# Kernel tuning notes

Measured on AMD Instinct MI355X. Metric: run time of the kernel, lower is better.

Reference implementation:

```python
import jax, jax.numpy as jnp
import numpy as np

E = 8          # num_experts
D = 512        # embed_dim
FF = 4         # ff_mult
H = D * FF     # hidden
B, N = 4, 2048
TOP_K = 2


def setup_inputs() -> dict:
    key = jax.random.key(0)
    ks = jax.random.split(key, 6)
    tokens = jax.random.normal(ks[0], (B, N, D), dtype=jnp.float32)
    # token-choice top-k routing: logits -> top-2 experts per token
    logits = jax.random.normal(ks[1], (B, N, E), dtype=jnp.float32)
    topv, topi = jax.lax.top_k(logits, TOP_K)            # (B,N,K)
    disp = jnp.zeros((B, N, E), jnp.float32)
    disp = jnp.take_along_axis(disp, topi, axis=-1)  # placeholder shape trick avoided below
    disp = jnp.zeros((B, N, E), jnp.float32).at[
        jnp.arange(B)[:, None, None], jnp.arange(N)[None, :, None], topi
    ].set(1.0)                                            # (B,N,E) 0/1 dispatch mask
    w = jax.nn.softmax(topv, axis=-1)                     # combine weights over selected
    comb = jnp.zeros((B, N, E), jnp.float32).at[
        jnp.arange(B)[:, None, None], jnp.arange(N)[None, :, None], topi
    ].set(w)
    # expert params (xavier-ish scale); out_proj gain 0.02 as in module init
    Wg = jax.random.normal(ks[2], (E, D, H), dtype=jnp.float32) * (2.0 / (D + H)) ** 0.5
    Wv = jax.random.normal(ks[3], (E, D, H), dtype=jnp.float32) * (2.0 / (D + H)) ** 0.5
    Wo = jax.random.normal(ks[4], (E, H, D), dtype=jnp.float32) * 0.02 * (2.0 / (D + H)) ** 0.5
    scales = jnp.full((E,), 1.0 / E, dtype=jnp.float32)   # output_scale per expert
    return {"tokens": tokens, "dispatch_weights": disp, "combine_weights": comb,
            "Wg": Wg, "Wv": Wv, "Wo": Wo, "scales": scales}


def reference(tokens, dispatch_weights, combine_weights, Wg, Wv, Wo, scales):
    """ExpertPool.forward: per-expert SwiGLU FFN, combined by routing weights.

    Dense-masked formulation (same math as gather->FFN->weighted scatter-add:
    expert outputs only contribute where dispatch>0).
    """
    b, n, d = tokens.shape
    x = tokens.reshape(b * n, d)                          # (M, D)
    gate = jax.nn.gelu(jnp.einsum('md,edh->emh', x, Wg), approximate=False)
    value = jnp.einsum('md,edh->emh', x, Wv)
    out_e = jnp.einsum('emh,ehd->emd', gate * value, Wo) * scales[:, None, None]
    mask = dispatch_weights.reshape(b * n, -1) > 0        # (M, E)
    w = jnp.where(mask, combine_weights.reshape(b * n, -1), 0.0)
    out = jnp.einsum('emd,me->md', out_e, w)              # weighted combine
    return out.reshape(b, n, d)
```

## Files before the change

### kernel.cpp

```cpp
#include <hip/hip_runtime.h>
#include <hip/hip_bf16.h>


#define NEXP 8
#define DIM 512
#define HID 2048
#define MTOK 8192
#define PMAX (2*MTOK)
#define TM 128
#define MT 144

typedef __bf16 bf16;
typedef __bf16 bf16x8 __attribute__((ext_vector_type(8)));
typedef float  f32x4  __attribute__((ext_vector_type(4)));

#define WAITVM(N) asm volatile("s_waitcnt vmcnt(" #N ")" ::: "memory")
#define SCHED0    __builtin_amdgcn_sched_barrier(0)
#define BAR       __builtin_amdgcn_s_barrier

__device__ __forceinline__ void gload16(const bf16* g, bf16* l) {
  __builtin_amdgcn_global_load_lds(
      (const __attribute__((address_space(1))) void*)g,
      (__attribute__((address_space(3))) void*)l, 16, 0, 0);
}

__global__ __launch_bounds__(256) void k_cvt_x(const float* __restrict__ in,
                                               bf16* __restrict__ out, int n4) {
  int i = blockIdx.x*256 + threadIdx.x;
  if (i >= n4) return;
  float4 v = ((const float4* __restrict__)in)[i];
  bf16 o[4];
  o[0]=(bf16)v.x; o[1]=(bf16)v.y; o[2]=(bf16)v.z; o[3]=(bf16)v.w;
  *(uint2*)&out[(size_t)i*4] = *(uint2*)o;
}

__global__ __launch_bounds__(256) void k_tcvt2(const float* __restrict__ in0,
                                               const float* __restrict__ in1,
                                               bf16* __restrict__ out0,
                                               bf16* __restrict__ out1, int R, int C) {
  __shared__ __align__(16) bf16 t[64][72];
  const int z = blockIdx.z;
  const int e = z & (NEXP-1);
  const float* __restrict__ pin = ((z < NEXP) ? in0 : in1) + (size_t)e*R*C;
  bf16* __restrict__ pout = ((z < NEXP) ? out0 : out1) + (size_t)e*R*C;
  const int c0 = blockIdx.x*64, r0 = blockIdx.y*64;
  const int tid = threadIdx.x;
  const int rr = tid>>4, cc4 = (tid&15)*4;
#pragma unroll
  for (int i=0;i<4;i++){
    int r = i*16 + rr;
    float4 v = *(const float4*)&pin[(size_t)(r0+r)*C + c0 + cc4];
    t[cc4+0][r]=(bf16)v.x; t[cc4+1][r]=(bf16)v.y;
    t[cc4+2][r]=(bf16)v.z; t[cc4+3][r]=(bf16)v.w;
  }
  __syncthreads();
#pragma unroll
  for (int i=0;i<4;i++){
    int c = i*16 + rr;
    *(uint2*)&pout[(size_t)(c0+c)*R + r0 + cc4] = *(uint2*)&t[c][cc4];
  }
}

__global__ __launch_bounds__(256) void k_count(const float* __restrict__ disp,
                                               int* __restrict__ cnt) {
  __shared__ int lc[NEXP];
  int t = threadIdx.x;
  if (t < NEXP) lc[t] = 0;
  __syncthreads();
  int m = blockIdx.x*256 + t;
  float4 d0 = *(const float4*)&disp[(size_t)m*NEXP];
  float4 d1 = *(const float4*)&disp[(size_t)m*NEXP+4];
  if (d0.x>0.f) atomicAdd(&lc[0],1);
  if (d0.y>0.f) atomicAdd(&lc[1],1);
  if (d0.z>0.f) atomicAdd(&lc[2],1);
  if (d0.w>0.f) atomicAdd(&lc[3],1);
  if (d1.x>0.f) atomicAdd(&lc[4],1);
  if (d1.y>0.f) atomicAdd(&lc[5],1);
  if (d1.z>0.f) atomicAdd(&lc[6],1);
  if (d1.w>0.f) atomicAdd(&lc[7],1);
  __syncthreads();
  if (t < NEXP) atomicAdd(&cnt[t], lc[t]);
}

__global__ void k_scan(const int* __restrict__ cnt, int* __restrict__ base,
                       int* __restrict__ te, int* __restrict__ trow, int* __restrict__ tn) {
  __shared__ int sb[NEXP+1], st[NEXP+1], sc[NEXP];
  if (threadIdx.x == 0){
    int b=0, t=0;
    for (int e=0;e<NEXP;e++){
      sb[e]=b; st[e]=t; sc[e]=cnt[e]; base[e]=b;
      b += sc[e];
      t += (sc[e]+TM-1)/TM;
    }
    sb[NEXP]=b; st[NEXP]=t;
  }
  __syncthreads();
  for (int idx=threadIdx.x; idx<MT; idx+=blockDim.x){
    int e=-1;
#pragma unroll
    for (int q=0;q<NEXP;q++) if (idx>=st[q] && idx<st[q+1]) e=q;
    if (e>=0){
      int k = idx - st[e];
      int nr = sc[e] - k*TM; if (nr>TM) nr=TM;
      te[idx]=e; trow[idx]=sb[e]+k*TM; tn[idx]=nr;
    } else te[idx]=-1;
  }
}

__global__ __launch_bounds__(256) void k_fill(const float* __restrict__ disp,
    const float* __restrict__ comb, const float* __restrict__ scales,
    const int* __restrict__ base, int* __restrict__ fillc,
    int* __restrict__ stok, float* __restrict__ sw, int* __restrict__ sslot) {
  int m = blockIdx.x*256 + threadIdx.x;
  int jj = 0;
#pragma unroll
  for (int e=0;e<NEXP;e++){
    float dv = disp[(size_t)m*NEXP + e];
    if (dv > 0.f) {
      int s = atomicAdd(&fillc[e], 1);
      int g = base[e] + s;
      stok[g] = m;
      sw[g] = comb[(size_t)m*NEXP + e] * scales[e];
      if (jj < 2) sslot[m*2 + jj] = g;
      jj++;
    }
  }
}

__global__ __launch_bounds__(256) void k_gemm1(const bf16* __restrict__ Xb,
    const bf16* __restrict__ WgT, const bf16* __restrict__ WvT,
    const int* __restrict__ te, const int* __restrict__ trow, const int* __restrict__ tn,
    const int* __restrict__ stok, bf16* __restrict__ H1) {
  const int tile = blockIdx.y;
  const int e = te[tile];
  if (e < 0) return;
  const int row0 = trow[tile], nrows = tn[tile];
  const int n0 = blockIdx.x*64;
  __shared__ __align__(16) bf16 Al[2*128*32];
  __shared__ __align__(16) bf16 Bgl[2*64*32];
  __shared__ __align__(16) bf16 Bvl[2*64*32];
  const int tid = threadIdx.x, lane = tid&63;
  const int wr = (tid>>7)&1, wc = (tid>>6)&1;
  const bf16* __restrict__ wg = WgT + (size_t)e*HID*DIM;
  const bf16* __restrict__ wv = WvT + (size_t)e*HID*DIM;

  const bf16* asrc[2];
#pragma unroll
  for (int i=0;i<2;i++){
    int c = i*256 + tid;
    int r = c>>2, qs = (c&3) ^ ((r>>1)&3);
    int gr = (r < nrows) ? (row0 + r) : row0;
    asrc[i] = Xb + (size_t)stok[gr]*DIM + qs*8;
  }
  const bf16 *bsg, *bsv;
  {
    int r = tid>>2, qs = (tid&3) ^ ((r>>1)&3);
    size_t o = (size_t)(n0 + r)*DIM + qs*8;
    bsg = wg + o; bsv = wv + o;
  }
  const int wbase = (tid&192)*8;

  auto stage = [&](int bi, int kt){
    const int k0 = kt*32;
    gload16(asrc[0]+k0, Al + bi*4096 + wbase);
    gload16(asrc[1]+k0, Al + bi*4096 + 2048 + wbase);
    gload16(bsg+k0, Bgl + bi*2048 + wbase);
    gload16(bsv+k0, Bvl + bi*2048 + wbase);
  };

  f32x4 accg[4][2] = {}, accv[4][2] = {};
  const int r15 = lane&15;
  const int koff = ((lane>>4) ^ ((r15>>1)&3))*8;
  stage(0, 0);
  for (int kt=0; kt<DIM/32; ++kt){
    const int bi = kt&1;
    if (kt+1 < DIM/32){ stage(bi^1, kt+1); WAITVM(4); }
    else WAITVM(0);
    BAR(); SCHED0;
    bf16x8 a[4], bg[2], bv[2];
#pragma unroll
    for (int ni=0; ni<2; ni++){
      bg[ni] = *(const bf16x8*)&Bgl[bi*2048 + (wc*32 + ni*16 + r15)*32 + koff];
      bv[ni] = *(const bf16x8*)&Bvl[bi*2048 + (wc*32 + ni*16 + r15)*32 + koff];
    }
#pragma unroll
    for (int mi=0; mi<4; mi++)
      a[mi] = *(const bf16x8*)&Al[bi*4096 + (wr*64 + mi*16 + r15)*32 + koff];
#pragma unroll
    for (int mi=0; mi<4; mi++)
#pragma unroll
      for (int ni=0; ni<2; ni++){
        accg[mi][ni] = __builtin_amdgcn_mfma_f32_16x16x32_bf16(a[mi], bg[ni], accg[mi][ni], 0,0,0);
        accv[mi][ni] = __builtin_amdgcn_mfma_f32_16x16x32_bf16(a[mi], bv[ni], accv[mi][ni], 0,0,0);
      }
    BAR(); SCHED0;
  }
  const int cb = n0 + wc*32 + r15;
  const int rb = wr*64 + (lane>>4)*4;
#pragma unroll
  for (int mi=0; mi<4; mi++)
#pragma unroll
    for (int j=0; j<4; j++){
      int r = rb + mi*16 + j;
      if (r < nrows){
#pragma unroll
        for (int ni=0; ni<2; ni++){
          float g = accg[mi][ni][j], v = accv[mi][ni][j];
          float ge = 0.5f*g*(1.f + erff(g*0.70710678118654752f));
          H1[(size_t)(row0+r)*HID + cb + ni*16] = (bf16)(ge*v);
        }
      }
    }
}

__global__ __launch_bounds__(256) void k_gemm2(const bf16* __restrict__ H1,
    const bf16* __restrict__ WoT,
    const int* __restrict__ te, const int* __restrict__ trow, const int* __restrict__ tn,
    const float* __restrict__ sw, float* __restrict__ gout) {
  const int L = blockIdx.x;
  const int tile = (L&7)*18 + (L>>5);
  const int n0 = ((L>>3)&3)*128;
  const int e = te[tile];
  if (e < 0) return;
  const int row0 = trow[tile], nrows = tn[tile];
  __shared__ __align__(16) bf16 Al[2*TM*64];
  __shared__ __align__(16) bf16 Bl[2*TM*64];
  const int tid = threadIdx.x, lane = tid&63;
  const int wr = (tid>>7)&1, wc = (tid>>6)&1;
  const bf16* __restrict__ wo = WoT + (size_t)e*DIM*HID;

  const bf16 *asrc[4], *bsrc[4];
#pragma unroll
  for (int i=0;i<4;i++){
    int c = i*256 + tid;
    int r = c>>3, qs = (c&7) ^ (r&7);
    int ar = (r < nrows) ? (row0 + r) : row0;
    asrc[i] = H1 + (size_t)ar*HID + qs*8;
    bsrc[i] = wo + (size_t)(n0 + r)*HID + qs*8;
  }
  const int wbase = (tid&192)*8;

  auto stage = [&](int bi, int kt){
    const int k0 = kt*64;
#pragma unroll
    for (int i=0;i<4;i++){
      gload16(asrc[i]+k0, Al + bi*TM*64 + i*2048 + wbase);
      gload16(bsrc[i]+k0, Bl + bi*TM*64 + i*2048 + wbase);
    }
  };

  f32x4 acc[4][4] = {};
  const int rsw = (lane&7)<<3;
  stage(0, 0);
  for (int kt=0; kt<HID/64; ++kt){
    const int bi = kt&1;
    if (kt+1 < HID/64){ stage(bi^1, kt+1); WAITVM(8); }
    else WAITVM(0);
    BAR(); SCHED0;
#pragma unroll
    for (int ks=0; ks<2; ks++){
      const int kos = (ks*32 + (lane>>4)*8) ^ rsw;
      bf16x8 a[4], b[4];
#pragma unroll
      for (int ni=0; ni<4; ni++)
        b[ni] = *(const bf16x8*)&Bl[bi*TM*64 + (wc*64 + ni*16 + (lane&15))*64 + kos];
#pragma unroll
      for (int mi=0; mi<4; mi++)
        a[mi] = *(const bf16x8*)&Al[bi*TM*64 + (wr*64 + mi*16 + (lane&15))*64 + kos];
#pragma unroll
      for (int mi=0; mi<4; mi++)
#pragma unroll
        for (int ni=0; ni<4; ni++)
          acc[mi][ni] = __builtin_amdgcn_mfma_f32_16x16x32_bf16(a[mi], b[ni], acc[mi][ni], 0,0,0);
    }
    BAR(); SCHED0;
  }
  const int cb = n0 + wc*64 + (lane&15);
  const int rb = wr*64 + (lane>>4)*4;
#pragma unroll
  for (int mi=0; mi<4; mi++)
#pragma unroll
    for (int j=0; j<4; j++){
      int r = rb + mi*16 + j;
      if (r < nrows){
        int slot = row0 + r;
        float wgt = sw[slot];
        float* op = gout + (size_t)slot*DIM + cb;
#pragma unroll
        for (int ni=0; ni<4; ni++)
          op[ni*16] = acc[mi][ni][j] * wgt;
      }
    }
}

__global__ __launch_bounds__(256) void k_comb(const float* __restrict__ gout,
    const int* __restrict__ sslot, float* __restrict__ out) {
  int idx = blockIdx.x*256 + threadIdx.x;
  int m = idx >> 7, c4 = (idx & 127)*4;
  int s0 = sslot[m*2], s1 = sslot[m*2+1];
  float4 x = *(const float4*)&gout[(size_t)s0*DIM + c4];
  float4 y = *(const float4*)&gout[(size_t)s1*DIM + c4];
  x.x += y.x; x.y += y.y; x.z += y.z; x.w += y.w;
  *(float4*)&out[(size_t)m*DIM + c4] = x;
}

extern "C" void kernel_launch(void* const* d_in, const int* in_sizes, int n_in,
                              void* d_out, int out_size, void* d_ws, size_t ws_size,
                              hipStream_t stream) {
  const float* tokens = (const float*)d_in[0];
  const float* disp   = (const float*)d_in[1];
  const float* comb   = (const float*)d_in[2];
  const float* Wg     = (const float*)d_in[3];
  const float* Wv     = (const float*)d_in[4];
  const float* Wo     = (const float*)d_in[5];
  const float* scales = (const float*)d_in[6];
  float* out = (float*)d_out;

  size_t off = 0;
  char* wsb = (char*)d_ws;
  auto take = [&](size_t bytes)->char* {
    char* q = wsb + off; off += (bytes + 255) & ~(size_t)255; return q;
  };
  int*   cnt   = (int*)  take(NEXP*4);
  int*   basee = (int*)  take(NEXP*4);
  int*   fillc = (int*)  take(NEXP*4);
  int*   te    = (int*)  take(MT*4);
  int*   trow  = (int*)  take(MT*4);
  int*   tnr   = (int*)  take(MT*4);
  int*   stok  = (int*)  take((size_t)PMAX*4);
  float* sw    = (float*)take((size_t)PMAX*4);
  int*   sslot = (int*)  take((size_t)MTOK*2*4);
  bf16*  Xb    = (bf16*) take((size_t)MTOK*DIM*2);
  bf16*  WgT   = (bf16*) take((size_t)NEXP*DIM*HID*2);
  bf16*  WvT   = (bf16*) take((size_t)NEXP*DIM*HID*2);
  bf16*  WoT   = (bf16*) take((size_t)NEXP*DIM*HID*2);
  bf16*  H1    = (bf16*) take((size_t)PMAX*HID*2);
  float* gout  = (float*)WgT;
  (void)ws_size; (void)in_sizes; (void)n_in; (void)out_size;

  hipMemsetAsync(d_ws, 0, 768, stream);

  k_cvt_x<<<dim3((MTOK*DIM/4)/256), 256, 0, stream>>>(tokens, Xb, MTOK*DIM/4);
  k_tcvt2<<<dim3(HID/64, DIM/64, 2*NEXP), 256, 0, stream>>>(Wg, Wv, WgT, WvT, DIM, HID);
  k_tcvt2<<<dim3(DIM/64, HID/64, NEXP), 256, 0, stream>>>(Wo, Wo, WoT, WoT, HID, DIM);
  k_count<<<dim3(MTOK/256), 256, 0, stream>>>(disp, cnt);
  k_scan <<<1, 64, 0, stream>>>(cnt, basee, te, trow, tnr);
  k_fill <<<dim3(MTOK/256), 256, 0, stream>>>(disp, comb, scales, basee, fillc, stok, sw, sslot);
  k_gemm1<<<dim3(HID/64, MT), 256, 0, stream>>>(Xb, WgT, WvT, te, trow, tnr, stok, H1);
  k_gemm2<<<dim3(8*18*4), 256, 0, stream>>>(H1, WoT, te, trow, tnr, sw, gout);
  k_comb <<<dim3(MTOK*DIM/4/256), 256, 0, stream>>>(gout, sslot, out);
}
```

Measured before the change: 229.7 us.

## Use single-wave 64x32 tiles for gate/value GEMM and polynomial erf GELU

The first expert GEMM now runs one 64-lane wave per block on a 64-row by 32-column tile, so it needs no workgroup barriers, and it gets its own finer tile schedule (TM1=64) separate from the second GEMM's 128-row tiles. The aim is less barrier overhead, less padding waste on partial expert tiles, and more blocks to spread across CUs. The exact erff is replaced by an Abramowitz-Stegun polynomial with __expf, which cuts epilogue cost but carries about 1e-7 absolute erf error. Smaller tiles lower operand reuse, so weight traffic from global memory or L2 goes up.

```diff
diff --git a/kernel.cpp b/kernel.cpp
--- a/kernel.cpp
+++ b/kernel.cpp
@@ -7,8 +7,10 @@
 #define HID 2048
 #define MTOK 8192
 #define PMAX (2*MTOK)
-#define TM 128
-#define MT 144
+#define TM1 64
+#define MT1 264
+#define TM2 128
+#define MT2 144
 
 typedef __bf16 bf16;
 typedef __bf16 bf16x8 __attribute__((ext_vector_type(8)));
@@ -22,6 +24,17 @@
   __builtin_amdgcn_global_load_lds(
       (const __attribute__((address_space(1))) void*)g,
       (__attribute__((address_space(3))) void*)l, 16, 0, 0);
+}
+
+__device__ __forceinline__ float gelu_f(float x){
+  float s = x * 0.70710678118654752f;
+  float a = fabsf(s);
+  float t = 1.0f / fmaf(0.3275911f, a, 1.0f);
+  float p = t*(0.254829592f + t*(-0.284496736f + t*(1.421413741f +
+            t*(-1.453152027f + t*1.061405429f))));
+  float er = 1.0f - p*__expf(-s*s);
+  er = copysignf(er, s);
+  return 0.5f*x*(1.0f + er);
 }
 
 __global__ __launch_bounds__(256) void k_cvt_x(const float* __restrict__ in,
@@ -83,27 +96,39 @@
 }
 
 __global__ void k_scan(const int* __restrict__ cnt, int* __restrict__ base,
-                       int* __restrict__ te, int* __restrict__ trow, int* __restrict__ tn) {
-  __shared__ int sb[NEXP+1], st[NEXP+1], sc[NEXP];
+                       int* __restrict__ te1, int* __restrict__ trow1, int* __restrict__ tn1,
+                       int* __restrict__ te2, int* __restrict__ trow2, int* __restrict__ tn2) {
+  __shared__ int sb[NEXP+1], st1[NEXP+1], st2[NEXP+1], sc[NEXP];
   if (threadIdx.x == 0){
-    int b=0, t=0;
+    int b=0, t1=0, t2=0;
     for (int e=0;e<NEXP;e++){
-      sb[e]=b; st[e]=t; sc[e]=cnt[e]; base[e]=b;
+      sb[e]=b; st1[e]=t1; st2[e]=t2; sc[e]=cnt[e]; base[e]=b;
       b += sc[e];
-      t += (sc[e]+TM-1)/TM;
-    }
-    sb[NEXP]=b; st[NEXP]=t;
+      t1 += (sc[e]+TM1-1)/TM1;
+      t2 += (sc[e]+TM2-1)/TM2;
+    }
+    sb[NEXP]=b; st1[NEXP]=t1; st2[NEXP]=t2;
   }
   __syncthreads();
-  for (int idx=threadIdx.x; idx<MT; idx+=blockDim.x){
+  for (int idx=threadIdx.x; idx<MT1; idx+=blockDim.x){
     int e=-1;
 #pragma unroll
-    for (int q=0;q<NEXP;q++) if (idx>=st[q] && idx<st[q+1]) e=q;
+    for (int q=0;q<NEXP;q++) if (idx>=st1[q] && idx<st1[q+1]) e=q;
     if (e>=0){
-      int k = idx - st[e];
-      int nr = sc[e] - k*TM; if (nr>TM) nr=TM;
-      te[idx]=e; trow[idx]=sb[e]+k*TM; tn[idx]=nr;
-    } else te[idx]=-1;
+      int k = idx - st1[e];
+      int nr = sc[e] - k*TM1; if (nr>TM1) nr=TM1;
+      te1[idx]=e; trow1[idx]=sb[e]+k*TM1; tn1[idx]=nr;
+    } else te1[idx]=-1;
+  }
+  for (int idx=threadIdx.x; idx<MT2; idx+=blockDim.x){
+    int e=-1;
+#pragma unroll
+    for (int q=0;q<NEXP;q++) if (idx>=st2[q] && idx<st2[q+1]) e=q;
+    if (e>=0){
+      int k = idx - st2[e];
+      int nr = sc[e] - k*TM2; if (nr>TM2) nr=TM2;
+      te2[idx]=e; trow2[idx]=sb[e]+k*TM2; tn2[idx]=nr;
+    } else te2[idx]=-1;
   }
 }
 
@@ -127,7 +152,7 @@
   }
 }
 
-__global__ __launch_bounds__(256) void k_gemm1(const bf16* __restrict__ Xb,
+__global__ __launch_bounds__(64) void k_gemm1(const bf16* __restrict__ Xb,
     const bf16* __restrict__ WgT, const bf16* __restrict__ WvT,
     const int* __restrict__ te, const int* __restrict__ trow, const int* __restrict__ tn,
     const int* __restrict__ stok, bf16* __restrict__ H1) {
@@ -135,79 +160,81 @@
   const int e = te[tile];
   if (e < 0) return;
   const int row0 = trow[tile], nrows = tn[tile];
-  const int n0 = blockIdx.x*64;
-  __shared__ __align__(16) bf16 Al[2*128*32];
-  __shared__ __align__(16) bf16 Bgl[2*64*32];
-  __shared__ __align__(16) bf16 Bvl[2*64*32];
-  const int tid = threadIdx.x, lane = tid&63;
-  const int wr = (tid>>7)&1, wc = (tid>>6)&1;
+  const int n0 = blockIdx.x*32;
+  __shared__ __align__(16) bf16 Al[2][2048];
+  __shared__ __align__(16) bf16 Bgl[2][1024];
+  __shared__ __align__(16) bf16 Bvl[2][1024];
+  const int lane = threadIdx.x;
   const bf16* __restrict__ wg = WgT + (size_t)e*HID*DIM;
   const bf16* __restrict__ wv = WvT + (size_t)e*HID*DIM;
 
-  const bf16* asrc[2];
-#pragma unroll
-  for (int i=0;i<2;i++){
-    int c = i*256 + tid;
+  const bf16* asrc[4];
+#pragma unroll
+  for (int i=0;i<4;i++){
+    int c = i*64 + lane;
     int r = c>>2, qs = (c&3) ^ ((r>>1)&3);
     int gr = (r < nrows) ? (row0 + r) : row0;
     asrc[i] = Xb + (size_t)stok[gr]*DIM + qs*8;
   }
-  const bf16 *bsg, *bsv;
-  {
-    int r = tid>>2, qs = (tid&3) ^ ((r>>1)&3);
+  const bf16 *bsg[2], *bsv[2];
+#pragma unroll
+  for (int j=0;j<2;j++){
+    int c = j*64 + lane;
+    int r = c>>2, qs = (c&3) ^ ((r>>1)&3);
     size_t o = (size_t)(n0 + r)*DIM + qs*8;
-    bsg = wg + o; bsv = wv + o;
-  }
-  const int wbase = (tid&192)*8;
+    bsg[j] = wg + o; bsv[j] = wv + o;
+  }
 
   auto stage = [&](int bi, int kt){
     const int k0 = kt*32;
-    gload16(asrc[0]+k0, Al + bi*4096 + wbase);
-    gload16(asrc[1]+k0, Al + bi*4096 + 2048 + wbase);
-    gload16(bsg+k0, Bgl + bi*2048 + wbase);
-    gload16(bsv+k0, Bvl + bi*2048 + wbase);
+#pragma unroll
+    for (int i=0;i<4;i++) gload16(asrc[i]+k0, &Al[bi][i*512]);
+#pragma unroll
+    for (int j=0;j<2;j++){
+      gload16(bsg[j]+k0, &Bgl[bi][j*512]);
+      gload16(bsv[j]+k0, &Bvl[bi][j*512]);
+    }
   };
 
-  f32x4 accg[4][2] = {}, accv[4][2] = {};
+  f32x4 ag[4][2] = {}, av[4][2] = {};
   const int r15 = lane&15;
   const int koff = ((lane>>4) ^ ((r15>>1)&3))*8;
+
   stage(0, 0);
   for (int kt=0; kt<DIM/32; ++kt){
     const int bi = kt&1;
-    if (kt+1 < DIM/32){ stage(bi^1, kt+1); WAITVM(4); }
+    if (kt+1 < DIM/32){ stage(bi^1, kt+1); WAITVM(8); }
     else WAITVM(0);
-    BAR(); SCHED0;
+    SCHED0;
     bf16x8 a[4], bg[2], bv[2];
 #pragma unroll
     for (int ni=0; ni<2; ni++){
-      bg[ni] = *(const bf16x8*)&Bgl[bi*2048 + (wc*32 + ni*16 + r15)*32 + koff];
-      bv[ni] = *(const bf16x8*)&Bvl[bi*2048 + (wc*32 + ni*16 + r15)*32 + koff];
+      bg[ni] = *(const bf16x8*)&Bgl[bi][(ni*16 + r15)*32 + koff];
+      bv[ni] = *(const bf16x8*)&Bvl[bi][(ni*16 + r15)*32 + koff];
     }
 #pragma unroll
     for (int mi=0; mi<4; mi++)
-      a[mi] = *(const bf16x8*)&Al[bi*4096 + (wr*64 + mi*16 + r15)*32 + koff];
+      a[mi] = *(const bf16x8*)&Al[bi][(mi*16 + r15)*32 + koff];
 #pragma unroll
     for (int mi=0; mi<4; mi++)
 #pragma unroll
       for (int ni=0; ni<2; ni++){
-        accg[mi][ni] = __builtin_amdgcn_mfma_f32_16x16x32_bf16(a[mi], bg[ni], accg[mi][ni], 0,0,0);
-        accv[mi][ni] = __builtin_amdgcn_mfma_f32_16x16x32_bf16(a[mi], bv[ni], accv[mi][ni], 0,0,0);
+        ag[mi][ni] = __builtin_amdgcn_mfma_f32_16x16x32_bf16(a[mi], bg[ni], ag[mi][ni], 0,0,0);
+        av[mi][ni] = __builtin_amdgcn_mfma_f32_16x16x32_bf16(a[mi], bv[ni], av[mi][ni], 0,0,0);
       }
-    BAR(); SCHED0;
-  }
-  const int cb = n0 + wc*32 + r15;
-  const int rb = wr*64 + (lane>>4)*4;
+  }
+
+  const int rb = (lane>>4)*4;
 #pragma unroll
   for (int mi=0; mi<4; mi++)
 #pragma unroll
     for (int j=0; j<4; j++){
-      int r = rb + mi*16 + j;
+      int r = mi*16 + rb + j;
       if (r < nrows){
 #pragma unroll
         for (int ni=0; ni<2; ni++){
-          float g = accg[mi][ni][j], v = accv[mi][ni][j];
-          float ge = 0.5f*g*(1.f + erff(g*0.70710678118654752f));
-          H1[(size_t)(row0+r)*HID + cb + ni*16] = (bf16)(ge*v);
+          float g = ag[mi][ni][j], v = av[mi][ni][j];
+          H1[(size_t)(row0+r)*HID + n0 + ni*16 + r15] = (bf16)(gelu_f(g)*v);
         }
       }
     }
@@ -223,8 +250,8 @@
   const int e = te[tile];
   if (e < 0) return;
   const int row0 = trow[tile], nrows = tn[tile];
-  __shared__ __align__(16) bf16 Al[2*TM*64];
-  __shared__ __align__(16) bf16 Bl[2*TM*64];
+  __shared__ __align__(16) bf16 Al[2*TM2*64];
+  __shared__ __align__(16) bf16 Bl[2*TM2*64];
   const int tid = threadIdx.x, lane = tid&63;
   const int wr = (tid>>7)&1, wc = (tid>>6)&1;
   const bf16* __restrict__ wo = WoT + (size_t)e*DIM*HID;
@@ -244,8 +271,8 @@
     const int k0 = kt*64;
 #pragma unroll
     for (int i=0;i<4;i++){
-      gload16(asrc[i]+k0, Al + bi*TM*64 + i*2048 + wbase);
-      gload16(bsrc[i]+k0, Bl + bi*TM*64 + i*2048 + wbase);
+      gload16(asrc[i]+k0, Al + bi*TM2*64 + i*2048 + wbase);
+      gload16(bsrc[i]+k0, Bl + bi*TM2*64 + i*2048 + wbase);
     }
   };
 
@@ -263,10 +290,10 @@
       bf16x8 a[4], b[4];
 #pragma unroll
       for (int ni=0; ni<4; ni++)
-        b[ni] = *(const bf16x8*)&Bl[bi*TM*64 + (wc*64 + ni*16 + (lane&15))*64 + kos];
+        b[ni] = *(const bf16x8*)&Bl[bi*TM2*64 + (wc*64 + ni*16 + (lane&15))*64 + kos];
 #pragma unroll
       for (int mi=0; mi<4; mi++)
-        a[mi] = *(const bf16x8*)&Al[bi*TM*64 + (wr*64 + mi*16 + (lane&15))*64 + kos];
+        a[mi] = *(const bf16x8*)&Al[bi*TM2*64 + (wr*64 + mi*16 + (lane&15))*64 + kos];
 #pragma unroll
       for (int mi=0; mi<4; mi++)
 #pragma unroll
@@ -324,9 +351,12 @@
   int*   cnt   = (int*)  take(NEXP*4);
   int*   basee = (int*)  take(NEXP*4);
   int*   fillc = (int*)  take(NEXP*4);
-  int*   te    = (int*)  take(MT*4);
-  int*   trow  = (int*)  take(MT*4);
-  int*   tnr   = (int*)  take(MT*4);
+  int*   te1   = (int*)  take(MT1*4);
+  int*   trow1 = (int*)  take(MT1*4);
+  int*   tn1   = (int*)  take(MT1*4);
+  int*   te2   = (int*)  take(MT2*4);
+  int*   trow2 = (int*)  take(MT2*4);
+  int*   tn2   = (int*)  take(MT2*4);
   int*   stok  = (int*)  take((size_t)PMAX*4);
   float* sw    = (float*)take((size_t)PMAX*4);
   int*   sslot = (int*)  take((size_t)MTOK*2*4);
@@ -344,9 +374,9 @@
   k_tcvt2<<<dim3(HID/64, DIM/64, 2*NEXP), 256, 0, stream>>>(Wg, Wv, WgT, WvT, DIM, HID);
   k_tcvt2<<<dim3(DIM/64, HID/64, NEXP), 256, 0, stream>>>(Wo, Wo, WoT, WoT, HID, DIM);
   k_count<<<dim3(MTOK/256), 256, 0, stream>>>(disp, cnt);
-  k_scan <<<1, 64, 0, stream>>>(cnt, basee, te, trow, tnr);
+  k_scan <<<1, 64, 0, stream>>>(cnt, basee, te1, trow1, tn1, te2, trow2, tn2);
   k_fill <<<dim3(MTOK/256), 256, 0, stream>>>(disp, comb, scales, basee, fillc, stok, sw, sslot);
-  k_gemm1<<<dim3(HID/64, MT), 256, 0, stream>>>(Xb, WgT, WvT, te, trow, tnr, stok, H1);
-  k_gemm2<<<dim3(8*18*4), 256, 0, stream>>>(H1, WoT, te, trow, tnr, sw, gout);
+  k_gemm1<<<dim3(HID/32, MT1), 64, 0, stream>>>(Xb, WgT, WvT, te1, trow1, tn1, stok, H1);
+  k_gemm2<<<dim3(8*18*4), 256, 0, stream>>>(H1, WoT, te2, trow2, tn2, sw, gout);
   k_comb <<<dim3(MTOK*DIM/4/256), 256, 0, stream>>>(gout, sslot, out);
 }
```

Result: slower. 274.9 us (+19.7%).

## Remap gemm1 grid to interleave expert tiles, shrink gemm2 K-step to 32

Applied to the files above, without the earlier changes.

gemm1 now uses a 1-D grid whose block index is decoded so that consecutive blocks cycle across 8 tile groups, with the N-column index in the middle bits. The aim is to spread concurrently running blocks across experts and XCDs for better L2 reuse of weights. gemm2 switches from a 64-wide K stage to a 32-wide one, with matching swizzle and half the LDS per buffer. That should raise occupancy, at the cost of twice as many barriers and loop iterations.

```diff
diff --git a/kernel.cpp b/kernel.cpp
--- a/kernel.cpp
+++ b/kernel.cpp
@@ -131,11 +131,12 @@
     const bf16* __restrict__ WgT, const bf16* __restrict__ WvT,
     const int* __restrict__ te, const int* __restrict__ trow, const int* __restrict__ tn,
     const int* __restrict__ stok, bf16* __restrict__ H1) {
-  const int tile = blockIdx.y;
+  const int L = blockIdx.x;
+  const int tile = (L&7)*18 + (L>>8);
+  const int n0 = ((L>>3)&31)*64;
   const int e = te[tile];
   if (e < 0) return;
   const int row0 = trow[tile], nrows = tn[tile];
-  const int n0 = blockIdx.x*64;
   __shared__ __align__(16) bf16 Al[2*128*32];
   __shared__ __align__(16) bf16 Bgl[2*64*32];
   __shared__ __align__(16) bf16 Bvl[2*64*32];
@@ -223,17 +224,17 @@
   const int e = te[tile];
   if (e < 0) return;
   const int row0 = trow[tile], nrows = tn[tile];
-  __shared__ __align__(16) bf16 Al[2*TM*64];
-  __shared__ __align__(16) bf16 Bl[2*TM*64];
+  __shared__ __align__(16) bf16 Al[2*128*32];
+  __shared__ __align__(16) bf16 Bl[2*128*32];
   const int tid = threadIdx.x, lane = tid&63;
   const int wr = (tid>>7)&1, wc = (tid>>6)&1;
   const bf16* __restrict__ wo = WoT + (size_t)e*DIM*HID;
 
-  const bf16 *asrc[4], *bsrc[4];
-#pragma unroll
-  for (int i=0;i<4;i++){
+  const bf16 *asrc[2], *bsrc[2];
+#pragma unroll
+  for (int i=0;i<2;i++){
     int c = i*256 + tid;
-    int r = c>>3, qs = (c&7) ^ (r&7);
+    int r = c>>2, qs = (c&3) ^ ((r>>1)&3);
     int ar = (r < nrows) ? (row0 + r) : row0;
     asrc[i] = H1 + (size_t)ar*HID + qs*8;
     bsrc[i] = wo + (size_t)(n0 + r)*HID + qs*8;
@@ -241,41 +242,38 @@
   const int wbase = (tid&192)*8;
 
   auto stage = [&](int bi, int kt){
-    const int k0 = kt*64;
-#pragma unroll
-    for (int i=0;i<4;i++){
-      gload16(asrc[i]+k0, Al + bi*TM*64 + i*2048 + wbase);
-      gload16(bsrc[i]+k0, Bl + bi*TM*64 + i*2048 + wbase);
+    const int k0 = kt*32;
+#pragma unroll
+    for (int i=0;i<2;i++){
+      gload16(asrc[i]+k0, Al + bi*4096 + i*2048 + wbase);
+      gload16(bsrc[i]+k0, Bl + bi*4096 + i*2048 + wbase);
     }
   };
 
   f32x4 acc[4][4] = {};
-  const int rsw = (lane&7)<<3;
+  const int r15 = lane&15;
+  const int koff = ((lane>>4) ^ ((r15>>1)&3))*8;
   stage(0, 0);
-  for (int kt=0; kt<HID/64; ++kt){
+  for (int kt=0; kt<HID/32; ++kt){
     const int bi = kt&1;
-    if (kt+1 < HID/64){ stage(bi^1, kt+1); WAITVM(8); }
+    if (kt+1 < HID/32){ stage(bi^1, kt+1); WAITVM(4); }
     else WAITVM(0);
     BAR(); SCHED0;
-#pragma unroll
-    for (int ks=0; ks<2; ks++){
-      const int kos = (ks*32 + (lane>>4)*8) ^ rsw;
-      bf16x8 a[4], b[4];
+    bf16x8 a[4], b[4];
+#pragma unroll
+    for (int ni=0; ni<4; ni++)
+      b[ni] = *(const bf16x8*)&Bl[bi*4096 + (wc*64 + ni*16 + r15)*32 + koff];
+#pragma unroll
+    for (int mi=0; mi<4; mi++)
+      a[mi] = *(const bf16x8*)&Al[bi*4096 + (wr*64 + mi*16 + r15)*32 + koff];
+#pragma unroll
+    for (int mi=0; mi<4; mi++)
 #pragma unroll
       for (int ni=0; ni<4; ni++)
-        b[ni] = *(const bf16x8*)&Bl[bi*TM*64 + (wc*64 + ni*16 + (lane&15))*64 + kos];
-#pragma unroll
-      for (int mi=0; mi<4; mi++)
-        a[mi] = *(const bf16x8*)&Al[bi*TM*64 + (wr*64 + mi*16 + (lane&15))*64 + kos];
-#pragma unroll
-      for (int mi=0; mi<4; mi++)
-#pragma unroll
-        for (int ni=0; ni<4; ni++)
-          acc[mi][ni] = __builtin_amdgcn_mfma_f32_16x16x32_bf16(a[mi], b[ni], acc[mi][ni], 0,0,0);
-    }
+        acc[mi][ni] = __builtin_amdgcn_mfma_f32_16x16x32_bf16(a[mi], b[ni], acc[mi][ni], 0,0,0);
     BAR(); SCHED0;
   }
-  const int cb = n0 + wc*64 + (lane&15);
+  const int cb = n0 + wc*64 + r15;
   const int rb = wr*64 + (lane>>4)*4;
 #pragma unroll
   for (int mi=0; mi<4; mi++)
@@ -346,7 +344,7 @@
   k_count<<<dim3(MTOK/256), 256, 0, stream>>>(disp, cnt);
   k_scan <<<1, 64, 0, stream>>>(cnt, basee, te, trow, tnr);
   k_fill <<<dim3(MTOK/256), 256, 0, stream>>>(disp, comb, scales, basee, fillc, stok, sw, sslot);
-  k_gemm1<<<dim3(HID/64, MT), 256, 0, stream>>>(Xb, WgT, WvT, te, trow, tnr, stok, H1);
+  k_gemm1<<<dim3(8*18*32), 256, 0, stream>>>(Xb, WgT, WvT, te, trow, tnr, stok, H1);
   k_gemm2<<<dim3(8*18*4), 256, 0, stream>>>(H1, WoT, te, trow, tnr, sw, gout);
   k_comb <<<dim3(MTOK*DIM/4/256), 256, 0, stream>>>(gout, sslot, out);
 }
```

New measurement: 225.5 us. Within noise of the previous version (-1.8%).
